# Performance work log

Measured on AMD Instinct MI355X. Metric: run time of the kernel, lower is better.

Reference implementation:

```python
import jax, jax.numpy as jnp
import numpy as np

N_HEAD = 16
N_EMBD = 1024
BLOCK = 2048
B, T = 4, 2048


def setup_inputs() -> dict:
    key = jax.random.key(0)
    ks = jax.random.split(key, 5)
    scale = 1.0 / np.sqrt(N_EMBD)
    return {
        "x": jax.random.normal(ks[0], (B, T, N_EMBD), dtype=jnp.float32),
        "W_attn": jax.random.normal(ks[1], (N_EMBD, 3 * N_EMBD), dtype=jnp.float32) * scale,
        "b_attn": jax.random.normal(ks[2], (3 * N_EMBD,), dtype=jnp.float32) * 0.02,
        "W_proj": jax.random.normal(ks[3], (N_EMBD, N_EMBD), dtype=jnp.float32) * scale,
        "b_proj": jax.random.normal(ks[4], (N_EMBD,), dtype=jnp.float32) * 0.02,
    }


def reference(x, W_attn, b_attn, W_proj, b_proj):
    Bb, Tt, C = x.shape
    hd = C // N_HEAD
    qkv = x @ W_attn + b_attn                      # [B,T,3C]
    q, k, v = jnp.split(qkv, 3, axis=2)
    # [B,H,T,hd]
    q = q.reshape(Bb, Tt, N_HEAD, hd).transpose(0, 2, 1, 3)
    k = k.reshape(Bb, Tt, N_HEAD, hd).transpose(0, 2, 1, 3)
    v = v.reshape(Bb, Tt, N_HEAD, hd).transpose(0, 2, 1, 3)
    att = jnp.einsum('bhqd,bhkd->bhqk', q, k) / np.sqrt(hd).astype(x.dtype)
    causal = jnp.tril(jnp.ones((Tt, Tt), dtype=bool))
    att = jnp.where(causal[None, None], att, jnp.finfo(att.dtype).min)
    att = jax.nn.softmax(att, axis=-1)
    y = jnp.einsum('bhqk,bhkd->bhqd', att, v)      # [B,H,T,hd]
    y = y.transpose(0, 2, 1, 3).reshape(Bb, Tt, C)
    return y @ W_proj + b_proj
```

## Files before the change

### kernel.cpp

```cpp
#include <hip/hip_runtime.h>
#include <stdint.h>

typedef unsigned short u16;
typedef __bf16 bf16;
typedef bf16 bf16x8 __attribute__((ext_vector_type(8)));
typedef float f32x4 __attribute__((ext_vector_type(4)));
typedef u16 u16x8 __attribute__((ext_vector_type(8)));
typedef u16 u16x4 __attribute__((ext_vector_type(4)));

#define T_SEQ 2048
#define NHEAD 16
#define HD    64
#define CEMB  1024
#define QS    8388608
#define QSCALE 0.18033688011112042f

__device__ __forceinline__ u16 f2b(float f){
  bf16 h = (bf16)f;
  return __builtin_bit_cast(u16, h);
}
__device__ __forceinline__ void glds16(const void* g, const void* l){
  __builtin_amdgcn_global_load_lds(
    (__attribute__((address_space(1))) unsigned int*)(uintptr_t)g,
    (__attribute__((address_space(3))) unsigned int*)(uintptr_t)l,
    16, 0, 0);
}

__global__ __launch_bounds__(256) void prep_kernel(
    const float* __restrict__ x, u16* __restrict__ xb,
    const float* __restrict__ Wa, u16* __restrict__ Wta,
    const float* __restrict__ Wp, u16* __restrict__ Wtp)
{
  __shared__ __align__(16) u16 tile[64][72];
  const int bid = blockIdx.x;
  const int tid = threadIdx.x;
  if (bid < 4096){
    const int i = (bid * 256 + tid) * 8;
    f32x4 a = *(const f32x4*)&x[i];
    f32x4 b = *(const f32x4*)&x[i + 4];
    u16x8 h;
    #pragma unroll
    for (int j = 0; j < 4; j++){ h[j] = f2b(a[j]); h[4+j] = f2b(b[j]); }
    *(u16x8*)&xb[i] = h;
    return;
  }
  const float* src; u16* dst; int K, N, bx, by;
  if (bid < 4864){ const int j = bid - 4096; src = Wa; dst = Wta; K = 1024; N = 3072; bx = j % 48; by = j / 48; }
  else           { const int j = bid - 4864; src = Wp; dst = Wtp; K = 1024; N = 1024; bx = j % 16; by = j / 16; }
  const int n0 = bx * 64, k0 = by * 64;
  #pragma unroll
  for (int it = 0; it < 4; it++){
    const int idx = it * 256 + tid;
    const int row = idx >> 4, c4 = (idx & 15) * 4;
    f32x4 v = *(const f32x4*)&src[(size_t)(k0 + row) * N + n0 + c4];
    #pragma unroll
    for (int j = 0; j < 4; j++) tile[row][c4 + j] = f2b(v[j]);
  }
  __syncthreads();
  const int r = tid >> 3, cc = (tid & 7) * 8;
  #pragma unroll
  for (int i = 0; i < 2; i++){
    const int rr = r + i * 32;
    u16x8 v;
    #pragma unroll
    for (int j = 0; j < 8; j++) v[j] = tile[cc + j][rr];
    *(u16x8*)&dst[(size_t)(n0 + rr) * K + k0 + cc] = v;
  }
}

template<int MODE>
__global__ __launch_bounds__(256) void gemm_bt(
    const u16* __restrict__ A, const u16* __restrict__ Bt,
    const float* __restrict__ bias, void* __restrict__ outraw, int Ktot)
{
  __shared__ __align__(16) u16 As[128*64];
  __shared__ __align__(16) u16 Bs[128*64];
  const int tid = threadIdx.x;
  const int lane = tid & 63, wave = tid >> 6;
  const int l15 = lane & 15, l4 = lane >> 4;
  const int wm = wave >> 1, wn = wave & 1;
  const int m0 = blockIdx.y * 128, n0 = blockIdx.x * 128;

  f32x4 acc[4][4] = {};

  for (int k0 = 0; k0 < Ktot; k0 += 64){
    #pragma unroll
    for (int ii = 0; ii < 4; ii++){
      const int slot0 = (wave*4 + ii) * 64;
      const int s = slot0 + lane;
      const int row = s >> 3;
      const int c = (s & 7) ^ (row & 7);
      glds16(&A [(size_t)(m0 + row) * Ktot + k0 + c*8], &As[slot0*8]);
      glds16(&Bt[(size_t)(n0 + row) * Ktot + k0 + c*8], &Bs[slot0*8]);
    }
    __syncthreads();
    #pragma unroll
    for (int ks = 0; ks < 2; ks++){
      bf16x8 af[4], bfr[4];
      #pragma unroll
      for (int mt = 0; mt < 4; mt++){
        const int rf = wm*64 + mt*16 + l15;
        const int slot = rf*8 + ((ks*4 + l4) ^ (rf & 7));
        af[mt] = *(const bf16x8*)&As[slot*8];
      }
      #pragma unroll
      for (int nt = 0; nt < 4; nt++){
        const int rf = wn*64 + nt*16 + l15;
        const int slot = rf*8 + ((ks*4 + l4) ^ (rf & 7));
        bfr[nt] = *(const bf16x8*)&Bs[slot*8];
      }
      #pragma unroll
      for (int mt = 0; mt < 4; mt++)
        #pragma unroll
        for (int nt = 0; nt < 4; nt++)
          acc[mt][nt] = __builtin_amdgcn_mfma_f32_16x16x32_bf16(
              af[mt], bfr[nt], acc[mt][nt], 0, 0, 0);
    }
    __syncthreads();
  }

  #pragma unroll
  for (int nt = 0; nt < 4; nt++){
    const int n = n0 + wn*64 + nt*16 + l15;
    const float bias_v = bias[n];
    if (MODE == 0){
      u16* out = (u16*)outraw;
      const int which = n >> 10;
      const int cc = n & 1023;
      const int h = cc >> 6, d = cc & 63;
      const float sc = (which == 0) ? QSCALE : 1.0f;
      if (which == 2){
        #pragma unroll
        for (int mt = 0; mt < 4; mt++){
          const int rowg = m0 + wm*64 + mt*16 + l4*4;
          const int bb = rowg >> 11, t = rowg & 2047;
          u16x4 pk;
          #pragma unroll
          for (int r = 0; r < 4; r++) pk[r] = f2b(acc[mt][nt][r] + bias_v);
          *(u16x4*)&out[(size_t)2*QS + ((size_t)(bb*NHEAD + h)*HD + d)*T_SEQ + t] = pk;
        }
      } else {
        #pragma unroll
        for (int mt = 0; mt < 4; mt++)
          #pragma unroll
          for (int r = 0; r < 4; r++){
            const int rowg = m0 + wm*64 + mt*16 + l4*4 + r;
            const int bb = rowg >> 11, t = rowg & 2047;
            out[(size_t)which*QS + ((size_t)(bb*NHEAD + h)*T_SEQ + t)*HD + d]
                = f2b((acc[mt][nt][r] + bias_v) * sc);
          }
      }
    } else {
      float* out = (float*)outraw;
      #pragma unroll
      for (int mt = 0; mt < 4; mt++)
        #pragma unroll
        for (int r = 0; r < 4; r++){
          const int rowg = m0 + wm*64 + mt*16 + l4*4 + r;
          out[(size_t)rowg*CEMB + n] = acc[mt][nt][r] + bias_v;
        }
    }
  }
}

__global__ __launch_bounds__(256, 4) void attn_kernel(
    const u16* __restrict__ qb, const u16* __restrict__ kb,
    const u16* __restrict__ vtb, u16* __restrict__ y)
{
  __shared__ __align__(16) u16 Ks[64*64];
  __shared__ __align__(16) u16 Vt[64*64];
  __shared__ __align__(16) u16 Pw[8*16*72];
  const int tid = threadIdx.x;
  const int lane = tid & 63, wave = tid >> 6;
  const int l15 = lane & 15, l4 = lane >> 4;
  const int qt = 15 - (blockIdx.x >> 6);
  const int bh = blockIdx.x & 63;
  const int q0 = qt * 128;
  const size_t base = (size_t)bh * (T_SEQ * HD);
  const u16* qp  = qb  + base;
  const u16* kp  = kb  + base;
  const u16* vtp = vtb + base;

  const int qmin0 = q0 + wave*32;
  const int qmin1 = qmin0 + 16;

  bf16x8 qf[2][2];
  #pragma unroll
  for (int g = 0; g < 2; g++){
    const int m = qmin0 + g*16 + l15;
    qf[g][0] = *(const bf16x8*)&qp[m*HD +      l4*8];
    qf[g][1] = *(const bf16x8*)&qp[m*HD + 32 + l4*8];
  }
  f32x4 o[2][4] = {};
  float l_run[2] = {0.f, 0.f};

  const int s0i = (wave*2 + 0) * 64 + lane;
  const int s1i = (wave*2 + 1) * 64 + lane;
  const int row0 = s0i >> 3, c0 = (s0i & 7) ^ (row0 & 7);
  const int row1 = s1i >> 3, c1 = (s1i & 7) ^ (row1 & 7);
  const int koff0 = row0*HD + c0*8, koff1 = row1*HD + c1*8;
  const int voff0 = row0*T_SEQ + c0*8, voff1 = row1*T_SEQ + c1*8;
  const int ldso0 = (wave*2 + 0) * 64 * 8, ldso1 = (wave*2 + 1) * 64 * 8;

  const int nkt = 2*qt + 2;
  for (int kt = 0; kt < nkt; kt++){
    __syncthreads();
    glds16(&kp [kt*4096 + koff0], &Ks[ldso0]);
    glds16(&kp [kt*4096 + koff1], &Ks[ldso1]);
    glds16(&vtp[kt*64   + voff0], &Vt[ldso0]);
    glds16(&vtp[kt*64   + voff1], &Vt[ldso1]);
    __syncthreads();

    const int t0 = kt*64;
    if (t0 <= qmin1 + 15){
      const bool act0 = (t0 <= qmin0 + 15);

      f32x4 s0[4], s1[4];
      #pragma unroll
      for (int nb = 0; nb < 4; nb++){
        f32x4 a0 = {}, a1 = {};
        #pragma unroll
        for (int ks = 0; ks < 2; ks++){
          const int rf = nb*16 + l15;
          const int slot = rf*8 + ((ks*4 + l4) ^ (rf & 7));
          bf16x8 kf = *(const bf16x8*)&Ks[slot*8];
          a1 = __builtin_amdgcn_mfma_f32_16x16x32_bf16(kf, qf[1][ks], a1, 0, 0, 0);
          if (act0)
            a0 = __builtin_amdgcn_mfma_f32_16x16x32_bf16(kf, qf[0][ks], a0, 0, 0, 0);
        }
        s1[nb] = a1; s0[nb] = a0;
      }

      #pragma unroll
      for (int g = 0; g < 2; g++){
        if (g == 0 && !act0) continue;
        f32x4* sf = (g == 0) ? s0 : s1;
        const int qmin = (g == 0) ? qmin0 : qmin1;
        const int qg = qmin + l15;
        float lsum = 0.f;
        if (t0 + 63 > qmin){
          #pragma unroll
          for (int nb = 0; nb < 4; nb++){
            u16x4 pk;
            #pragma unroll
            for (int r = 0; r < 4; r++){
              const int t = t0 + nb*16 + l4*4 + r;
              float p = __builtin_amdgcn_exp2f(sf[nb][r]);
              p = (t <= qg) ? p : 0.0f;
              lsum += p;
              pk[r] = f2b(p);
            }
            *(u16x4*)&Pw[(wave*2 + g)*1152 + l15*72 + nb*16 + l4*4] = pk;
          }
        } else {
          #pragma unroll
          for (int nb = 0; nb < 4; nb++){
            u16x4 pk;
            #pragma unroll
            for (int r = 0; r < 4; r++){
              const float p = __builtin_amdgcn_exp2f(sf[nb][r]);
              lsum += p;
              pk[r] = f2b(p);
            }
            *(u16x4*)&Pw[(wave*2 + g)*1152 + l15*72 + nb*16 + l4*4] = pk;
          }
        }
        l_run[g] += lsum;
      }

      #pragma unroll
      for (int ks = 0; ks < 2; ks++){
        bf16x8 pf1 = *(const bf16x8*)&Pw[(wave*2 + 1)*1152 + l15*72 + ks*32 + l4*8];
        bf16x8 pf0;
        if (act0) pf0 = *(const bf16x8*)&Pw[(wave*2 + 0)*1152 + l15*72 + ks*32 + l4*8];
        #pragma unroll
        for (int nh = 0; nh < 4; nh++){
          const int rf = nh*16 + l15;
          const int slot = rf*8 + ((ks*4 + l4) ^ (rf & 7));
          bf16x8 vf = *(const bf16x8*)&Vt[slot*8];
          o[1][nh] = __builtin_amdgcn_mfma_f32_16x16x32_bf16(vf, pf1, o[1][nh], 0, 0, 0);
          if (act0)
            o[0][nh] = __builtin_amdgcn_mfma_f32_16x16x32_bf16(vf, pf0, o[0][nh], 0, 0, 0);
        }
      }
    }
  }

  const int b = bh >> 4, h = bh & 15;
  #pragma unroll
  for (int g = 0; g < 2; g++){
    float lr = l_run[g];
    lr += __shfl_xor(lr, 16);
    lr += __shfl_xor(lr, 32);
    const float inv_l = 1.0f / lr;
    const int t = qmin0 + g*16 + l15;
    #pragma unroll
    for (int nh = 0; nh < 4; nh++){
      u16x4 pk;
      #pragma unroll
      for (int r = 0; r < 4; r++) pk[r] = f2b(o[g][nh][r] * inv_l);
      *(u16x4*)&y[((size_t)(b*T_SEQ + t))*CEMB + h*HD + nh*16 + l4*4] = pk;
    }
  }
}

extern "C" void kernel_launch(void* const* d_in, const int* in_sizes, int n_in,
                              void* d_out, int out_size, void* d_ws, size_t ws_size,
                              hipStream_t stream) {
  const float* x      = (const float*)d_in[0];
  const float* W_attn = (const float*)d_in[1];
  const float* b_attn = (const float*)d_in[2];
  const float* W_proj = (const float*)d_in[3];
  const float* b_proj = (const float*)d_in[4];
  float* out = (float*)d_out;
  u16* ws  = (u16*)d_ws;

  u16* Wt_attn = ws;
  u16* Wt_proj = ws + 3145728;
  u16* xb      = ws + 4194304;
  u16* qkv     = ws + 12582912;
  u16* y       = xb;

  prep_kernel<<<5120, 256, 0, stream>>>(x, xb, W_attn, Wt_attn, W_proj, Wt_proj);
  gemm_bt<0><<<dim3(24, 64), 256, 0, stream>>>(xb, Wt_attn, b_attn, qkv, 1024);
  attn_kernel<<<1024, 256, 0, stream>>>(qkv, qkv + QS, qkv + 2*QS, y);
  gemm_bt<1><<<dim3(8, 64), 256, 0, stream>>>(y, Wt_proj, b_proj, out, 1024);
}
```

Baseline: 244.1 us.

## Add 256x256-tile QKV GEMM with double-buffered direct-to-LDS loads

Replaces the 128x128 QKV projection GEMM with a new 512-thread kernel that computes 256x256 output tiles. It double-buffers swizzled global-to-LDS loads across a 128 KB LDS footprint and interleaves staging of the next K-slices with MFMA quadrants, using explicit barriers and waitcnts plus s_setprio around the MFMA blocks. The goal is more data reuse per tile and better overlap of memory traffic with matrix math. The cost is much higher LDS use and a grid of only 384 blocks, which may leave some CUs idle. It also makes an odd no-op edit to the old gemm_bt indexing.

```diff
diff --git a/kernel.cpp b/kernel.cpp
--- a/kernel.cpp
+++ b/kernel.cpp
@@ -68,6 +68,170 @@
   }
 }
 
+
+#define BARRIER() asm volatile("s_barrier" ::: "memory")
+#define WAITV(N)  asm volatile("s_waitcnt vmcnt(" #N ")" ::: "memory")
+#define WAITL0()  asm volatile("s_waitcnt lgkmcnt(0)" ::: "memory")
+
+#define STAGE_A(KT, H) do{ \
+  const size_t _g = (size_t)(H)*128*(size_t)Ktot + (size_t)(KT)*64; \
+  char* _dst = ldsb + ((((KT)&1)*2+(H))<<14) + woff; \
+  glds16(asrc0 + _g, _dst); \
+  glds16(asrc1 + _g, _dst + 8192); \
+}while(0)
+
+#define STAGE_B(KT, H) do{ \
+  const size_t _g = (size_t)(H)*128*(size_t)Ktot + (size_t)(KT)*64; \
+  char* _dst = ldsb + 65536 + ((((KT)&1)*2+(H))<<14) + woff; \
+  glds16(bsrc0 + _g, _dst); \
+  glds16(bsrc1 + _g, _dst + 8192); \
+}while(0)
+
+#define LDA(D, QM) do{ \
+  const char* _b = ldsb + (((D)*2+(QM))<<14) + arf; \
+  _Pragma("unroll") \
+  for (int mt = 0; mt < 4; mt++){ \
+    af[mt][0] = *(const bf16x8*)(_b + mt*2048 + k0off); \
+    af[mt][1] = *(const bf16x8*)(_b + mt*2048 + k1off); \
+  } \
+}while(0)
+
+#define LDB(DST, D, QN) do{ \
+  const char* _b = ldsb + 65536 + (((D)*2+(QN))<<14) + brf; \
+  _Pragma("unroll") \
+  for (int nt = 0; nt < 2; nt++){ \
+    DST[nt][0] = *(const bf16x8*)(_b + nt*2048 + k0off); \
+    DST[nt][1] = *(const bf16x8*)(_b + nt*2048 + k1off); \
+  } \
+}while(0)
+
+#define MFMA_QUAD(QM, QN, BF) do{ \
+  __builtin_amdgcn_s_setprio(1); \
+  _Pragma("unroll") \
+  for (int ks = 0; ks < 2; ks++){ \
+    _Pragma("unroll") \
+    for (int mt = 0; mt < 4; mt++){ \
+      _Pragma("unroll") \
+      for (int nt = 0; nt < 2; nt++){ \
+        acc[QM][mt][QN][nt] = __builtin_amdgcn_mfma_f32_16x16x32_bf16( \
+            af[mt][ks], BF[nt][ks], acc[QM][mt][QN][nt], 0, 0, 0); \
+      } \
+    } \
+  } \
+  __builtin_amdgcn_s_setprio(0); \
+}while(0)
+
+__global__ __launch_bounds__(512, 2) void gemm_qkv(
+    const u16* __restrict__ A, const u16* __restrict__ Bt,
+    const float* __restrict__ bias, u16* __restrict__ out, int Ktot)
+{
+  __shared__ __align__(16) char lds_s[131072];
+  char* ldsb = lds_s;
+  const int tid = threadIdx.x;
+  const int lane = tid & 63, wave = tid >> 6;
+  const int l15 = lane & 15, l4 = lane >> 4;
+  const int wm = wave >> 2, wn = wave & 3;
+  const int m0 = blockIdx.y * 256, n0 = blockIdx.x * 256;
+  const int NT = Ktot >> 6;
+  const int woff = wave * 1024;
+
+  int grow0, gcol0, grow1, gcol1;
+  { const int P = tid*16;        const int L = P ^ (((P>>9)&1)<<5); grow0 = L>>7; gcol0 = (L&127)>>1; }
+  { const int P = 8192 + tid*16; const int L = P ^ (((P>>9)&1)<<5); grow1 = L>>7; gcol1 = (L&127)>>1; }
+  const u16* asrc0 = A  + (size_t)(m0 + grow0)*Ktot + gcol0;
+  const u16* asrc1 = A  + (size_t)(m0 + grow1)*Ktot + gcol1;
+  const u16* bsrc0 = Bt + (size_t)(n0 + grow0)*Ktot + gcol0;
+  const u16* bsrc1 = Bt + (size_t)(n0 + grow1)*Ktot + gcol1;
+
+  const int sw = ((l15 >> 2) & 1) << 5;
+  const int k0off = (l4*16) ^ sw;
+  const int k1off = (64 + l4*16) ^ sw;
+  const int arf = (wm*64 + l15) * 128;
+  const int brf = (wn*32 + l15) * 128;
+
+  f32x4 acc[2][4][2][2] = {};
+
+  STAGE_A(0,0); STAGE_B(0,0); STAGE_A(0,1); STAGE_B(0,1);
+  STAGE_A(1,0); STAGE_B(1,0);
+  WAITV(4);
+  BARRIER();
+
+  for (int c = 0; c < NT; c++){
+    const int d = c & 1;
+    bf16x8 af[4][2], b0[2][2], b1[2][2];
+
+    LDA(d, 0);
+    LDB(b0, d, 0);
+    if (c+1 < NT) STAGE_A(c+1, 1);
+    BARRIER();
+    WAITL0();
+    MFMA_QUAD(0, 0, b0);
+    BARRIER();
+
+    LDB(b1, d, 1);
+    if (c+1 < NT) STAGE_B(c+1, 1);
+    BARRIER();
+    WAITL0();
+    MFMA_QUAD(0, 1, b1);
+    BARRIER();
+
+    LDA(d, 1);
+    if (c+2 < NT) STAGE_A(c+2, 0);
+    BARRIER();
+    WAITL0();
+    MFMA_QUAD(1, 0, b0);
+    BARRIER();
+
+    if (c+2 < NT) STAGE_B(c+2, 0);
+    BARRIER();
+    MFMA_QUAD(1, 1, b1);
+    if (c == NT-2)      WAITV(0);
+    else if (c < NT-2)  WAITV(4);
+    BARRIER();
+  }
+
+  const int which = n0 >> 10;
+  #pragma unroll
+  for (int qn = 0; qn < 2; qn++){
+    #pragma unroll
+    for (int nt = 0; nt < 2; nt++){
+      const int n = n0 + qn*128 + wn*32 + nt*16 + l15;
+      const float bias_v = bias[n];
+      const int cc = n & 1023;
+      const int h = cc >> 6, dd = cc & 63;
+      if (which == 2){
+        #pragma unroll
+        for (int qm = 0; qm < 2; qm++){
+          #pragma unroll
+          for (int mt = 0; mt < 4; mt++){
+            const int rowg = m0 + qm*128 + wm*64 + mt*16 + l4*4;
+            const int bb = rowg >> 11, t = rowg & 2047;
+            u16x4 pk;
+            #pragma unroll
+            for (int r = 0; r < 4; r++) pk[r] = f2b(acc[qm][mt][qn][nt][r] + bias_v);
+            *(u16x4*)&out[(size_t)2*QS + ((size_t)(bb*NHEAD + h)*HD + dd)*T_SEQ + t] = pk;
+          }
+        }
+      } else {
+        const float sc = (which == 0) ? QSCALE : 1.0f;
+        #pragma unroll
+        for (int qm = 0; qm < 2; qm++){
+          #pragma unroll
+          for (int mt = 0; mt < 4; mt++){
+            #pragma unroll
+            for (int r = 0; r < 4; r++){
+              const int rowg = m0 + qm*128 + wm*64 + mt*16 + l4*4 + r;
+              const int bb = rowg >> 11, t = rowg & 2047;
+              out[(size_t)which*QS + ((size_t)(bb*NHEAD + h)*T_SEQ + t)*HD + dd]
+                  = f2b((acc[qm][mt][qn][nt][r] + bias_v) * sc);
+            }
+          }
+        }
+      }
+    }
+  }
+}
+
 template<int MODE>
 __global__ __launch_bounds__(256) void gemm_bt(
     const u16* __restrict__ A, const u16* __restrict__ Bt,
@@ -146,7 +310,7 @@
           for (int r = 0; r < 4; r++){
             const int rowg = m0 + wm*64 + mt*16 + l4*4 + r;
             const int bb = rowg >> 11, t = rowg & 2047;
-            out[(size_t)which*QS + ((size_t)(bb*NHEAD + h)*T_SEQ + t)*HD + d]
+            out[(size_t)which*QS + ((size_t)(bb*NHEAD + t)*0 + (bb*NHEAD + h)*T_SEQ + t)*HD + d]
                 = f2b((acc[mt][nt][r] + bias_v) * sc);
           }
       }
@@ -322,7 +486,7 @@
   u16* y       = xb;
 
   prep_kernel<<<5120, 256, 0, stream>>>(x, xb, W_attn, Wt_attn, W_proj, Wt_proj);
-  gemm_bt<0><<<dim3(24, 64), 256, 0, stream>>>(xb, Wt_attn, b_attn, qkv, 1024);
+  gemm_qkv<<<dim3(12, 32), 512, 0, stream>>>(xb, Wt_attn, b_attn, qkv, 1024);
   attn_kernel<<<1024, 256, 0, stream>>>(qkv, qkv + QS, qkv + 2*QS, y);
   gemm_bt<1><<<dim3(8, 64), 256, 0, stream>>>(y, Wt_proj, b_proj, out, 1024);
 }
```

Measured after the change: 252.9 us. 1.04x slower.

## Double-buffer K/V tiles in attention with async global-to-LDS prefetch

Applied to the files above, without the earlier changes.

The attention kernel now keeps two LDS buffers for K and V^T and issues the global_load_lds for tile kt+1 before computing on tile kt. It waits on vmcnt and uses raw s_barrier instead of two __syncthreads per iteration. This hides the load latency of each tile behind the MFMA work on the previous one. The cost is doubled LDS use, so occupancy is lowered from 4 to 3 blocks via launch bounds. The templated GEMM is split into two plain kernels with no behavioural change.

```diff
diff --git a/kernel.cpp b/kernel.cpp
--- a/kernel.cpp
+++ b/kernel.cpp
@@ -14,6 +14,9 @@
 #define CEMB  1024
 #define QS    8388608
 #define QSCALE 0.18033688011112042f
+
+#define BARRIER() asm volatile("s_barrier" ::: "memory")
+#define WAITV(N)  asm volatile("s_waitcnt vmcnt(" #N ")" ::: "memory")
 
 __device__ __forceinline__ u16 f2b(float f){
   bf16 h = (bf16)f;
@@ -68,10 +71,9 @@
   }
 }
 
-template<int MODE>
-__global__ __launch_bounds__(256) void gemm_bt(
+__global__ __launch_bounds__(256) void gemm_qkv128(
     const u16* __restrict__ A, const u16* __restrict__ Bt,
-    const float* __restrict__ bias, void* __restrict__ outraw, int Ktot)
+    const float* __restrict__ bias, u16* __restrict__ out, int Ktot)
 {
   __shared__ __align__(16) u16 As[128*64];
   __shared__ __align__(16) u16 Bs[128*64];
@@ -123,52 +125,104 @@
   for (int nt = 0; nt < 4; nt++){
     const int n = n0 + wn*64 + nt*16 + l15;
     const float bias_v = bias[n];
-    if (MODE == 0){
-      u16* out = (u16*)outraw;
-      const int which = n >> 10;
-      const int cc = n & 1023;
-      const int h = cc >> 6, d = cc & 63;
-      const float sc = (which == 0) ? QSCALE : 1.0f;
-      if (which == 2){
-        #pragma unroll
-        for (int mt = 0; mt < 4; mt++){
-          const int rowg = m0 + wm*64 + mt*16 + l4*4;
-          const int bb = rowg >> 11, t = rowg & 2047;
-          u16x4 pk;
-          #pragma unroll
-          for (int r = 0; r < 4; r++) pk[r] = f2b(acc[mt][nt][r] + bias_v);
-          *(u16x4*)&out[(size_t)2*QS + ((size_t)(bb*NHEAD + h)*HD + d)*T_SEQ + t] = pk;
-        }
-      } else {
-        #pragma unroll
-        for (int mt = 0; mt < 4; mt++)
-          #pragma unroll
-          for (int r = 0; r < 4; r++){
-            const int rowg = m0 + wm*64 + mt*16 + l4*4 + r;
-            const int bb = rowg >> 11, t = rowg & 2047;
-            out[(size_t)which*QS + ((size_t)(bb*NHEAD + h)*T_SEQ + t)*HD + d]
-                = f2b((acc[mt][nt][r] + bias_v) * sc);
-          }
+    const int which = n >> 10;
+    const int cc = n & 1023;
+    const int h = cc >> 6, d = cc & 63;
+    const float sc = (which == 0) ? QSCALE : 1.0f;
+    if (which == 2){
+      #pragma unroll
+      for (int mt = 0; mt < 4; mt++){
+        const int rowg = m0 + wm*64 + mt*16 + l4*4;
+        const int bb = rowg >> 11, t = rowg & 2047;
+        u16x4 pk;
+        #pragma unroll
+        for (int r = 0; r < 4; r++) pk[r] = f2b(acc[mt][nt][r] + bias_v);
+        *(u16x4*)&out[(size_t)2*QS + ((size_t)(bb*NHEAD + h)*HD + d)*T_SEQ + t] = pk;
       }
     } else {
-      float* out = (float*)outraw;
       #pragma unroll
       for (int mt = 0; mt < 4; mt++)
         #pragma unroll
         for (int r = 0; r < 4; r++){
           const int rowg = m0 + wm*64 + mt*16 + l4*4 + r;
-          out[(size_t)rowg*CEMB + n] = acc[mt][nt][r] + bias_v;
+          const int bb = rowg >> 11, t = rowg & 2047;
+          out[(size_t)which*QS + ((size_t)(bb*NHEAD + h)*T_SEQ + t)*HD + d]
+              = f2b((acc[mt][nt][r] + bias_v) * sc);
         }
     }
   }
 }
 
-__global__ __launch_bounds__(256, 4) void attn_kernel(
+__global__ __launch_bounds__(256) void gemm_proj(
+    const u16* __restrict__ A, const u16* __restrict__ Bt,
+    const float* __restrict__ bias, float* __restrict__ out, int Ktot)
+{
+  __shared__ __align__(16) u16 As[128*64];
+  __shared__ __align__(16) u16 Bs[128*64];
+  const int tid = threadIdx.x;
+  const int lane = tid & 63, wave = tid >> 6;
+  const int l15 = lane & 15, l4 = lane >> 4;
+  const int wm = wave >> 1, wn = wave & 1;
+  const int m0 = blockIdx.y * 128, n0 = blockIdx.x * 128;
+
+  f32x4 acc[4][4] = {};
+
+  for (int k0 = 0; k0 < Ktot; k0 += 64){
+    #pragma unroll
+    for (int ii = 0; ii < 4; ii++){
+      const int slot0 = (wave*4 + ii) * 64;
+      const int s = slot0 + lane;
+      const int row = s >> 3;
+      const int c = (s & 7) ^ (row & 7);
+      glds16(&A [(size_t)(m0 + row) * Ktot + k0 + c*8], &As[slot0*8]);
+      glds16(&Bt[(size_t)(n0 + row) * Ktot + k0 + c*8], &Bs[slot0*8]);
+    }
+    __syncthreads();
+    #pragma unroll
+    for (int ks = 0; ks < 2; ks++){
+      bf16x8 af[4], bfr[4];
+      #pragma unroll
+      for (int mt = 0; mt < 4; mt++){
+        const int rf = wm*64 + mt*16 + l15;
+        const int slot = rf*8 + ((ks*4 + l4) ^ (rf & 7));
+        af[mt] = *(const bf16x8*)&As[slot*8];
+      }
+      #pragma unroll
+      for (int nt = 0; nt < 4; nt++){
+        const int rf = wn*64 + nt*16 + l15;
+        const int slot = rf*8 + ((ks*4 + l4) ^ (rf & 7));
+        bfr[nt] = *(const bf16x8*)&Bs[slot*8];
+      }
+      #pragma unroll
+      for (int mt = 0; mt < 4; mt++)
+        #pragma unroll
+        for (int nt = 0; nt < 4; nt++)
+          acc[mt][nt] = __builtin_amdgcn_mfma_f32_16x16x32_bf16(
+              af[mt], bfr[nt], acc[mt][nt], 0, 0, 0);
+    }
+    __syncthreads();
+  }
+
+  #pragma unroll
+  for (int nt = 0; nt < 4; nt++){
+    const int n = n0 + wn*64 + nt*16 + l15;
+    const float bias_v = bias[n];
+    #pragma unroll
+    for (int mt = 0; mt < 4; mt++)
+      #pragma unroll
+      for (int r = 0; r < 4; r++){
+        const int rowg = m0 + wm*64 + mt*16 + l4*4 + r;
+        out[(size_t)rowg*CEMB + n] = acc[mt][nt][r] + bias_v;
+      }
+  }
+}
+
+__global__ __launch_bounds__(256, 3) void attn_kernel(
     const u16* __restrict__ qb, const u16* __restrict__ kb,
     const u16* __restrict__ vtb, u16* __restrict__ y)
 {
-  __shared__ __align__(16) u16 Ks[64*64];
-  __shared__ __align__(16) u16 Vt[64*64];
+  __shared__ __align__(16) u16 Ks[2*64*64];
+  __shared__ __align__(16) u16 Vt[2*64*64];
   __shared__ __align__(16) u16 Pw[8*16*72];
   const int tid = threadIdx.x;
   const int lane = tid & 63, wave = tid >> 6;
@@ -203,13 +257,25 @@
   const int ldso0 = (wave*2 + 0) * 64 * 8, ldso1 = (wave*2 + 1) * 64 * 8;
 
   const int nkt = 2*qt + 2;
+
+  glds16(&kp [koff0], &Ks[ldso0]);
+  glds16(&kp [koff1], &Ks[ldso1]);
+  glds16(&vtp[voff0], &Vt[ldso0]);
+  glds16(&vtp[voff1], &Vt[ldso1]);
+
   for (int kt = 0; kt < nkt; kt++){
-    __syncthreads();
-    glds16(&kp [kt*4096 + koff0], &Ks[ldso0]);
-    glds16(&kp [kt*4096 + koff1], &Ks[ldso1]);
-    glds16(&vtp[kt*64   + voff0], &Vt[ldso0]);
-    glds16(&vtp[kt*64   + voff1], &Vt[ldso1]);
-    __syncthreads();
+    const int cb = (kt & 1) * 4096;
+    if (kt + 1 < nkt){
+      const int nb = ((kt + 1) & 1) * 4096;
+      glds16(&kp [(kt+1)*4096 + koff0], &Ks[nb + ldso0]);
+      glds16(&kp [(kt+1)*4096 + koff1], &Ks[nb + ldso1]);
+      glds16(&vtp[(kt+1)*64   + voff0], &Vt[nb + ldso0]);
+      glds16(&vtp[(kt+1)*64   + voff1], &Vt[nb + ldso1]);
+      WAITV(4);
+    } else {
+      WAITV(0);
+    }
+    BARRIER();
 
     const int t0 = kt*64;
     if (t0 <= qmin1 + 15){
@@ -217,18 +283,18 @@
 
       f32x4 s0[4], s1[4];
       #pragma unroll
-      for (int nb = 0; nb < 4; nb++){
+      for (int nb2 = 0; nb2 < 4; nb2++){
         f32x4 a0 = {}, a1 = {};
         #pragma unroll
         for (int ks = 0; ks < 2; ks++){
-          const int rf = nb*16 + l15;
+          const int rf = nb2*16 + l15;
           const int slot = rf*8 + ((ks*4 + l4) ^ (rf & 7));
-          bf16x8 kf = *(const bf16x8*)&Ks[slot*8];
+          bf16x8 kf = *(const bf16x8*)&Ks[cb + slot*8];
           a1 = __builtin_amdgcn_mfma_f32_16x16x32_bf16(kf, qf[1][ks], a1, 0, 0, 0);
           if (act0)
             a0 = __builtin_amdgcn_mfma_f32_16x16x32_bf16(kf, qf[0][ks], a0, 0, 0, 0);
         }
-        s1[nb] = a1; s0[nb] = a0;
+        s1[nb2] = a1; s0[nb2] = a0;
       }
 
       #pragma unroll
@@ -240,29 +306,29 @@
         float lsum = 0.f;
         if (t0 + 63 > qmin){
           #pragma unroll
-          for (int nb = 0; nb < 4; nb++){
+          for (int nb2 = 0; nb2 < 4; nb2++){
             u16x4 pk;
             #pragma unroll
             for (int r = 0; r < 4; r++){
-              const int t = t0 + nb*16 + l4*4 + r;
-              float p = __builtin_amdgcn_exp2f(sf[nb][r]);
+              const int t = t0 + nb2*16 + l4*4 + r;
+              float p = __builtin_amdgcn_exp2f(sf[nb2][r]);
               p = (t <= qg) ? p : 0.0f;
               lsum += p;
               pk[r] = f2b(p);
             }
-            *(u16x4*)&Pw[(wave*2 + g)*1152 + l15*72 + nb*16 + l4*4] = pk;
+            *(u16x4*)&Pw[(wave*2 + g)*1152 + l15*72 + nb2*16 + l4*4] = pk;
           }
         } else {
           #pragma unroll
-          for (int nb = 0; nb < 4; nb++){
+          for (int nb2 = 0; nb2 < 4; nb2++){
             u16x4 pk;
             #pragma unroll
             for (int r = 0; r < 4; r++){
-              const float p = __builtin_amdgcn_exp2f(sf[nb][r]);
+              const float p = __builtin_amdgcn_exp2f(sf[nb2][r]);
               lsum += p;
               pk[r] = f2b(p);
             }
-            *(u16x4*)&Pw[(wave*2 + g)*1152 + l15*72 + nb*16 + l4*4] = pk;
+            *(u16x4*)&Pw[(wave*2 + g)*1152 + l15*72 + nb2*16 + l4*4] = pk;
           }
         }
         l_run[g] += lsum;
@@ -277,13 +343,14 @@
         for (int nh = 0; nh < 4; nh++){
           const int rf = nh*16 + l15;
           const int slot = rf*8 + ((ks*4 + l4) ^ (rf & 7));
-          bf16x8 vf = *(const bf16x8*)&Vt[slot*8];
+          bf16x8 vf = *(const bf16x8*)&Vt[cb + slot*8];
           o[1][nh] = __builtin_amdgcn_mfma_f32_16x16x32_bf16(vf, pf1, o[1][nh], 0, 0, 0);
           if (act0)
             o[0][nh] = __builtin_amdgcn_mfma_f32_16x16x32_bf16(vf, pf0, o[0][nh], 0, 0, 0);
         }
       }
     }
+    BARRIER();
   }
 
   const int b = bh >> 4, h = bh & 15;
@@ -322,7 +389,7 @@
   u16* y       = xb;
 
   prep_kernel<<<5120, 256, 0, stream>>>(x, xb, W_attn, Wt_attn, W_proj, Wt_proj);
-  gemm_bt<0><<<dim3(24, 64), 256, 0, stream>>>(xb, Wt_attn, b_attn, qkv, 1024);
+  gemm_qkv128<<<dim3(24, 64), 256, 0, stream>>>(xb, Wt_attn, b_attn, qkv, 1024);
   attn_kernel<<<1024, 256, 0, stream>>>(qkv, qkv + QS, qkv + 2*QS, y);
-  gemm_bt<1><<<dim3(8, 64), 256, 0, stream>>>(y, Wt_proj, b_proj, out, 1024);
-}
+  gemm_proj<<<dim3(8, 64), 256, 0, stream>>>(y, Wt_proj, b_proj, out, 1024);
+}
```

Measured after the change: 238.1 us. -2.5%, faster.
